# Performance work log

Measured on AMD Instinct MI355X. Metric: run time of the kernel, lower is better.

Reference implementation:

```python
import jax, jax.numpy as jnp
import numpy as np

V, E, H = 100000, 50, 64   # vocab, embedding dim, GRU hidden
B, T = 1024, 200           # batch, max playlist length


def setup_inputs() -> dict:
    key = jax.random.key(0)
    ks = jax.random.split(key, 12)
    ids = jax.random.randint(ks[0], (B, T), 1, V)
    lengths = jax.random.randint(ks[1], (B,), T // 4, T + 1)
    pos = jnp.arange(T)[None, :]
    input_tracks = jnp.where(pos < lengths[:, None], ids, 0)  # 0 = pad (mask_zero)
    s = 0.05
    p = lambda k, shp: jax.random.normal(k, shp, dtype=jnp.float32) * s
    z = lambda shp: jnp.zeros(shp, jnp.float32)
    return {
        "input_tracks": input_tracks,
        "emb": p(ks[2], (V, E)),
        "Wx_f": p(ks[3], (E, 3 * H)), "Wh_f": p(ks[4], (H, 3 * H)),
        "bi_f": z(3 * H), "br_f": z(3 * H),
        "Wx_b": p(ks[5], (E, 3 * H)), "Wh_b": p(ks[6], (H, 3 * H)),
        "bi_b": z(3 * H), "br_b": z(3 * H),
        "Wk": p(ks[7], (2 * H, H)), "bk": z(H),
        "Wq": p(ks[8], (H, H)), "bq": z(H),
        "We": p(ks[9], (H, 1)), "be": z(1),
    }


def _gru(x, mask, Wx, Wh, bi, br):
    """Keras GRU (reset_after=True) with masking; masked steps carry state.
    x: [B,T,E] float, mask: [B,T] bool. Returns (outputs [B,T,H], final state [B,H])."""
    gx = jnp.einsum('bte,eh->bth', x, Wx) + bi  # precompute input projections [B,T,3H]

    def step(h, inp):
        gxt, mt = inp                     # [B,3H], [B]
        gh = h @ Wh + br                  # [B,3H] recurrent projections (with recurrent bias)
        xz, xr, xh = jnp.split(gxt, 3, axis=-1)
        hz, hr, hn = jnp.split(gh, 3, axis=-1)
        zg = jax.nn.sigmoid(xz + hz)
        rg = jax.nn.sigmoid(xr + hr)
        hh = jnp.tanh(xh + rg * hn)
        h_new = zg * h + (1.0 - zg) * hh
        h_new = jnp.where(mt[:, None], h_new, h)  # carry state through padding
        return h_new, h_new

    h0 = jnp.zeros((x.shape[0], Wh.shape[0]), x.dtype)
    hT, outs = jax.lax.scan(step, h0, (gx.transpose(1, 0, 2), mask.T))
    return outs.transpose(1, 0, 2), hT


def reference(input_tracks, emb, Wx_f, Wh_f, bi_f, br_f, Wx_b, Wh_b, bi_b, br_b,
              Wk, bk, Wq, bq, We, be):
    mask = input_tracks != 0                       # [B,T]
    x = emb[input_tracks]                          # [B,T,E]
    out_f, h_f = _gru(x, mask, Wx_f, Wh_f, bi_f, br_f)
    out_b_rev, _ = _gru(x[:, ::-1], mask[:, ::-1], Wx_b, Wh_b, bi_b, br_b)
    out_b = out_b_rev[:, ::-1]
    out = jnp.concatenate([out_f, out_b], axis=-1)  # [B,T,2H]
    keys = out @ Wk + bk                            # [B,T,H]
    query = (h_f @ Wq + bq)[:, None, :]             # [B,1,H]
    energy = jnp.tanh(keys + query) @ We + be       # [B,T,1]
    energy = energy + (1.0 - mask.astype(jnp.float32))[:, :, None] * (-1e9)
    weights = jax.nn.softmax(energy, axis=1)        # softmax over time
    context = jnp.sum(weights * out, axis=1)        # [B,2H]
    return context
```

## Files before the change

### kernel.cpp

```cpp
#include <hip/hip_runtime.h>
#include <hip/hip_bf16.h>

#define VV 100000
#define EE 50
#define HH 64
#define BB 1024
#define TT 200

typedef float v4f __attribute__((ext_vector_type(4)));
typedef float f32x4 __attribute__((ext_vector_type(4)));
typedef short bf16x8 __attribute__((ext_vector_type(8)));
typedef _Float16 f16x8 __attribute__((ext_vector_type(8)));

__device__ __forceinline__ float fsig(float x) {
    return 1.f / (1.f + __expf(-x));
}
__device__ __forceinline__ float ftanh(float x) {
    float e = __expf(2.f * x);
    return 1.f - 2.f / (e + 1.f);
}
__device__ __forceinline__ short f2bf(float f) {
    union { float f; unsigned u; } v; v.f = f;
    unsigned r = v.u + 0x7FFFu + ((v.u >> 16) & 1u);
    return (short)(r >> 16);
}

__global__ __launch_bounds__(256) void embw_kernel(
    const float* __restrict__ emb,
    const float* __restrict__ Wx_f, const float* __restrict__ bi_f,
    const float* __restrict__ Wx_b, const float* __restrict__ bi_b,
    float* __restrict__ embW_f, float* __restrict__ embW_b)
{
    const float* Wx = blockIdx.y ? Wx_b : Wx_f;
    const float* bi = blockIdx.y ? bi_b : bi_f;
    float* embW     = blockIdx.y ? embW_b : embW_f;
    __shared__ float wx_lds[EE * 192];
    __shared__ float emb_lds[32 * EE];
    const int tid = threadIdx.x;
    const int v0 = blockIdx.x * 32;
    for (int i = tid; i < EE * 192; i += 256) wx_lds[i] = Wx[i];
    for (int i = tid; i < 32 * EE; i += 256) emb_lds[i] = emb[(size_t)v0 * EE + i];
    __syncthreads();
    const int cg = tid & 63;
    const int rg = tid >> 6;
    float acc[8][3];
    #pragma unroll
    for (int i = 0; i < 8; i++) {
        acc[i][0] = bi[cg];
        acc[i][1] = bi[cg + 64];
        acc[i][2] = bi[cg + 128];
    }
    for (int k = 0; k < EE; k++) {
        const float wx0 = wx_lds[k * 192 + cg];
        const float wx1 = wx_lds[k * 192 + cg + 64];
        const float wx2 = wx_lds[k * 192 + cg + 128];
        #pragma unroll
        for (int i = 0; i < 8; i++) {
            const float ev = emb_lds[(rg * 8 + i) * EE + k];
            acc[i][0] = fmaf(ev, wx0, acc[i][0]);
            acc[i][1] = fmaf(ev, wx1, acc[i][1]);
            acc[i][2] = fmaf(ev, wx2, acc[i][2]);
        }
    }
    #pragma unroll
    for (int i = 0; i < 8; i++) {
        const size_t row = (size_t)(v0 + rg * 8 + i) * 192;
        embW[row + cg]       = acc[i][0];
        embW[row + cg + 64]  = acc[i][1];
        embW[row + cg + 128] = acc[i][2];
    }
}

__global__ __launch_bounds__(256, 1) void gru8_kernel(
    const int* __restrict__ ids,
    const float* __restrict__ embW_f, const float* __restrict__ embW_b,
    const float* __restrict__ Wh_f, const float* __restrict__ br_f,
    const float* __restrict__ Wh_b, const float* __restrict__ br_b,
    float* __restrict__ outb,
    float* __restrict__ hf_out)
{
    const int tid  = threadIdx.x;
    const int w    = tid >> 6;
    const int lane = tid & 63;
    const int l15  = lane & 15;
    const int lhi  = lane >> 4;
    const int dir  = blockIdx.y;
    const int b0   = blockIdx.x * 16;
    const float* eW = dir ? embW_b : embW_f;
    const float* Wh = dir ? Wh_b : Wh_f;
    const float* br = dir ? br_b : br_f;
    const int c = 16 * w + l15;

    f16x8 bw[3][2];
    #pragma unroll
    for (int g = 0; g < 3; g++) {
        #pragma unroll
        for (int kt = 0; kt < 2; kt++) {
            #pragma unroll
            for (int jj = 0; jj < 8; jj++)
                bw[g][kt][jj] = (_Float16)Wh[(size_t)(32 * kt + 8 * lhi + jj) * 192 + 64 * g + c];
        }
    }
    const float brz = br[c], brr = br[64 + c], brn = br[128 + c];

    __shared__ __align__(16) _Float16 hlds[2][16][72];
    __shared__ int ids_s[16 * TT];
    for (int i = tid; i < 16 * TT; i += 256) ids_s[i] = ids[(size_t)b0 * TT + i];
    for (int i = tid; i < 2 * 16 * 72; i += 256) ((_Float16*)hlds)[i] = (_Float16)0.f;
    float hold[4] = {0.f, 0.f, 0.f, 0.f};
    __syncthreads();

    const int t0 = dir ? (TT - 1) : 0;
    const int dt = dir ? -1 : 1;

    int id0[4], id1[4];
    float gx0[3][4], gx1[3][4];
    #pragma unroll
    for (int r = 0; r < 4; r++) {
        id0[r] = ids_s[(4 * lhi + r) * TT + t0];
        id1[r] = ids_s[(4 * lhi + r) * TT + t0 + dt];
        const float* p0 = eW + (size_t)id0[r] * 192 + c;
        const float* p1 = eW + (size_t)id1[r] * 192 + c;
        #pragma unroll
        for (int g = 0; g < 3; g++) { gx0[g][r] = p0[64 * g]; gx1[g][r] = p1[64 * g]; }
    }

    int cur = 0;
    #pragma unroll 2
    for (int s = 0; s < TT; s++) {
        const int t = t0 + s * dt;
        int id2[4];
        float gx2[3][4];
        if (s + 2 < TT) {
            #pragma unroll
            for (int r = 0; r < 4; r++) {
                id2[r] = ids_s[(4 * lhi + r) * TT + t + 2 * dt];
                const float* p2 = eW + (size_t)id2[r] * 192 + c;
                #pragma unroll
                for (int g = 0; g < 3; g++) gx2[g][r] = p2[64 * g];
            }
        } else {
            #pragma unroll
            for (int r = 0; r < 4; r++) {
                id2[r] = 0;
                #pragma unroll
                for (int g = 0; g < 3; g++) gx2[g][r] = 0.f;
            }
        }
        const f16x8 a0 = *(const f16x8*)&hlds[cur][l15][8 * lhi];
        const f16x8 a1 = *(const f16x8*)&hlds[cur][l15][32 + 8 * lhi];
        f32x4 az = {0.f, 0.f, 0.f, 0.f};
        f32x4 ar = {0.f, 0.f, 0.f, 0.f};
        f32x4 an = {0.f, 0.f, 0.f, 0.f};
        az = __builtin_amdgcn_mfma_f32_16x16x32_f16(a0, bw[0][0], az, 0, 0, 0);
        ar = __builtin_amdgcn_mfma_f32_16x16x32_f16(a0, bw[1][0], ar, 0, 0, 0);
        an = __builtin_amdgcn_mfma_f32_16x16x32_f16(a0, bw[2][0], an, 0, 0, 0);
        az = __builtin_amdgcn_mfma_f32_16x16x32_f16(a1, bw[0][1], az, 0, 0, 0);
        ar = __builtin_amdgcn_mfma_f32_16x16x32_f16(a1, bw[1][1], ar, 0, 0, 0);
        an = __builtin_amdgcn_mfma_f32_16x16x32_f16(a1, bw[2][1], an, 0, 0, 0);
        #pragma unroll
        for (int r = 0; r < 4; r++) {
            const float z  = fsig(gx0[0][r] + az[r] + brz);
            const float rg = fsig(gx0[1][r] + ar[r] + brr);
            const float hh = ftanh(gx0[2][r] + rg * (an[r] + brn));
            float hnew = z * hold[r] + (1.f - z) * hh;
            hnew = (id0[r] != 0) ? hnew : hold[r];
            hold[r] = hnew;
            hlds[cur ^ 1][4 * lhi + r][c] = (_Float16)hnew;
            outb[((size_t)(b0 + 4 * lhi + r) * TT + t) * 128 + dir * 64 + c] = hnew;
        }
        cur ^= 1;
        asm volatile("s_waitcnt lgkmcnt(0)\n\ts_barrier" ::: "memory");
        #pragma unroll
        for (int r = 0; r < 4; r++) {
            id0[r] = id1[r]; id1[r] = id2[r];
            #pragma unroll
            for (int g = 0; g < 3; g++) { gx0[g][r] = gx1[g][r]; gx1[g][r] = gx2[g][r]; }
        }
    }
    if (dir == 0) {
        #pragma unroll
        for (int r = 0; r < 4; r++)
            hf_out[(size_t)(b0 + 4 * lhi + r) * 64 + c] = hold[r];
    }
}

#define NTILE 13

__global__ __launch_bounds__(256) void attn7_kernel(
    const int* __restrict__ ids,
    const float* __restrict__ outb,
    const float* __restrict__ hf,
    const float* __restrict__ Wk, const float* __restrict__ bk,
    const float* __restrict__ Wq, const float* __restrict__ bq,
    const float* __restrict__ We, const float* __restrict__ be,
    float* __restrict__ ctx)
{
    __shared__ __align__(16) short wk_sw[1024 * 8];
    __shared__ float q_lds[64];
    __shared__ float we_lds[64];
    __shared__ float e_lds[TT];
    __shared__ float part[4][128];
    const int b = blockIdx.x;
    const int tid = threadIdx.x;
    const int w = tid >> 6;
    const int lane = tid & 63;
    const int l15 = lane & 15;
    const int lhi = lane >> 4;

    #pragma unroll
    for (int i = 0; i < 4; i++) {
        const int slot = tid + 256 * i;
        const int s_l15 = slot & 15;
        const int s_nt  = (slot >> 4) & 3;
        const int s_lhi = (slot >> 6) & 3;
        const int s_ks  = slot >> 8;
        const int kbase = 32 * s_ks + 8 * s_lhi;
        const int col   = 16 * s_nt + s_l15;
        bf16x8 v;
        #pragma unroll
        for (int jj = 0; jj < 8; jj++) v[jj] = f2bf(Wk[(size_t)(kbase + jj) * 64 + col]);
        *(bf16x8*)&wk_sw[slot * 8] = v;
    }
    if (tid < 64) {
        float qc = bq[tid];
        const float* hfb = hf + (size_t)b * 64;
        for (int k = 0; k < 64; k++) qc = fmaf(hfb[k], Wq[k * 64 + tid], qc);
        q_lds[tid] = qc;
        we_lds[tid] = We[tid];
    }
    __syncthreads();

    for (int tile = w; tile < NTILE; tile += 4) {
        const int t0 = tile * 16;
        const int t = t0 + l15;
        f32x4 acc[4];
        #pragma unroll
        for (int nt = 0; nt < 4; nt++) { acc[nt][0] = 0.f; acc[nt][1] = 0.f; acc[nt][2] = 0.f; acc[nt][3] = 0.f; }
        #pragma unroll
        for (int ks = 0; ks < 4; ks++) {
            bf16x8 a;
            if (t < TT) {
                const float* p = outb + ((size_t)b * TT + t) * 128 + 32 * ks + 8 * lhi;
                const float4 lo = *(const float4*)p;
                const float4 hi = *(const float4*)(p + 4);
                a[0] = f2bf(lo.x); a[1] = f2bf(lo.y); a[2] = f2bf(lo.z); a[3] = f2bf(lo.w);
                a[4] = f2bf(hi.x); a[5] = f2bf(hi.y); a[6] = f2bf(hi.z); a[7] = f2bf(hi.w);
            } else {
                #pragma unroll
                for (int jj = 0; jj < 8; jj++) a[jj] = 0;
            }
            #pragma unroll
            for (int nt = 0; nt < 4; nt++) {
                const bf16x8 bf = *(const bf16x8*)&wk_sw[(ks * 256 + lhi * 64 + nt * 16 + l15) * 8];
                acc[nt] = __builtin_amdgcn_mfma_f32_16x16x32_bf16(a, bf, acc[nt], 0, 0, 0);
            }
        }
        float ep0 = 0.f, ep1 = 0.f, ep2 = 0.f, ep3 = 0.f;
        #pragma unroll
        for (int nt = 0; nt < 4; nt++) {
            const int c = 16 * nt + l15;
            const float qn = q_lds[c];
            const float wen = we_lds[c];
            ep0 = fmaf(wen, ftanh(acc[nt][0] + qn), ep0);
            ep1 = fmaf(wen, ftanh(acc[nt][1] + qn), ep1);
            ep2 = fmaf(wen, ftanh(acc[nt][2] + qn), ep2);
            ep3 = fmaf(wen, ftanh(acc[nt][3] + qn), ep3);
        }
        #pragma unroll
        for (int off = 1; off < 16; off <<= 1) {
            ep0 += __shfl_xor(ep0, off);
            ep1 += __shfl_xor(ep1, off);
            ep2 += __shfl_xor(ep2, off);
            ep3 += __shfl_xor(ep3, off);
        }
        if (l15 == 0) {
            const int rbase = t0 + 4 * lhi;
            if (rbase + 0 < TT) e_lds[rbase + 0] = ep0;
            if (rbase + 1 < TT) e_lds[rbase + 1] = ep1;
            if (rbase + 2 < TT) e_lds[rbase + 2] = ep2;
            if (rbase + 3 < TT) e_lds[rbase + 3] = ep3;
        }
    }
    __syncthreads();
    if (w == 0) {
        const float bev = be[0];
        for (int t = lane; t < TT; t += 64) {
            float e = e_lds[t] + bev;
            if (ids[(size_t)b * TT + t] == 0) e -= 1e9f;
            e_lds[t] = e;
        }
        float m = -1e30f;
        for (int t = lane; t < TT; t += 64) m = fmaxf(m, e_lds[t]);
        #pragma unroll
        for (int off = 32; off > 0; off >>= 1) m = fmaxf(m, __shfl_xor(m, off));
        float ssum = 0.f;
        for (int t = lane; t < TT; t += 64) { const float v = __expf(e_lds[t] - m); e_lds[t] = v; ssum += v; }
        #pragma unroll
        for (int off = 32; off > 0; off >>= 1) ssum += __shfl_xor(ssum, off);
        const float inv = 1.f / ssum;
        for (int t = lane; t < TT; t += 64) e_lds[t] *= inv;
    }
    __syncthreads();
    float c0 = 0.f, c1 = 0.f;
    for (int t = w; t < TT; t += 4) {
        const float* orow = outb + ((size_t)b * TT + t) * 128;
        const float wt = e_lds[t];
        c0 = fmaf(wt, orow[lane], c0);
        c1 = fmaf(wt, orow[64 + lane], c1);
    }
    part[w][lane] = c0;
    part[w][64 + lane] = c1;
    __syncthreads();
    if (tid < 128)
        ctx[(size_t)b * 128 + tid] = part[0][tid] + part[1][tid] + part[2][tid] + part[3][tid];
}

template<bool USE_EMBW>
__global__ __launch_bounds__(192, 2) void gru_kernel(
    const int* __restrict__ ids,
    const float* __restrict__ embW_f, const float* __restrict__ embW_b,
    const float* __restrict__ emb,
    const float* __restrict__ Wx_f, const float* __restrict__ bi_f,
    const float* __restrict__ Wx_b, const float* __restrict__ bi_b,
    const float* __restrict__ Wh_f, const float* __restrict__ br_f,
    const float* __restrict__ Wh_b, const float* __restrict__ br_b,
    float* __restrict__ outb, float* __restrict__ hf_out)
{
    constexpr int R = 4;
    __shared__ float h_lds[R][64];
    __shared__ float rg_lds[R][64];
    __shared__ float hh_lds[R][64];
    __shared__ int ids_lds[R * TT];
    const int tid = threadIdx.x;
    const int w = tid >> 6;
    const int j = tid & 63;
    const int dir = blockIdx.y;
    const int b0 = blockIdx.x * R;
    const float* embW = dir ? embW_b : embW_f;
    const float* Wh   = dir ? Wh_b : Wh_f;
    const float* br   = dir ? br_b : br_f;
    const float* Wx   = dir ? Wx_b : Wx_f;
    const float* bi   = dir ? bi_b : bi_f;
    const int c = w * 64 + j;

    float whc[64];
    #pragma unroll
    for (int k = 0; k < 64; k++) whc[k] = Wh[k * 192 + c];
    const float brc = br[c];
    float wxc[EE];
    float bic = 0.f;
    if (!USE_EMBW) {
        #pragma unroll
        for (int k = 0; k < EE; k++) wxc[k] = Wx[k * 192 + c];
        bic = bi[c];
    }
    for (int i = tid; i < R * TT; i += 192) ids_lds[i] = ids[(size_t)b0 * TT + i];
    if (w == 0) {
        #pragma unroll
        for (int r = 0; r < R; r++) h_lds[r][j] = 0.f;
    }
    __syncthreads();

    for (int s = 0; s < TT; s++) {
        const int t = dir ? (TT - 1 - s) : s;
        int idv[R];
        float gxv[R], accv[R];
        #pragma unroll
        for (int r = 0; r < R; r++) idv[r] = ids_lds[r * TT + t];
        if (USE_EMBW) {
            #pragma unroll
            for (int r = 0; r < R; r++) gxv[r] = embW[(size_t)idv[r] * 192 + c];
        } else {
            #pragma unroll
            for (int r = 0; r < R; r++) {
                float acc = bic;
                const float* er = emb + (size_t)idv[r] * EE;
                #pragma unroll
                for (int k = 0; k < EE; k++) acc = fmaf(er[k], wxc[k], acc);
                gxv[r] = acc;
            }
        }
        #pragma unroll
        for (int r = 0; r < R; r++) {
            float acc = brc;
            const float4* h4 = (const float4*)(&h_lds[r][0]);
            #pragma unroll
            for (int k4 = 0; k4 < 16; k4++) {
                const float4 hv = h4[k4];
                acc = fmaf(hv.x, whc[4 * k4 + 0], acc);
                acc = fmaf(hv.y, whc[4 * k4 + 1], acc);
                acc = fmaf(hv.z, whc[4 * k4 + 2], acc);
                acc = fmaf(hv.w, whc[4 * k4 + 3], acc);
            }
            accv[r] = acc;
        }
        float zg[R] = {};
        if (w == 1) {
            #pragma unroll
            for (int r = 0; r < R; r++) rg_lds[r][j] = fsig(gxv[r] + accv[r]);
        } else if (w == 0) {
            #pragma unroll
            for (int r = 0; r < R; r++) zg[r] = fsig(gxv[r] + accv[r]);
        }
        __syncthreads();
        if (w == 2) {
            #pragma unroll
            for (int r = 0; r < R; r++)
                hh_lds[r][j] = ftanh(gxv[r] + rg_lds[r][j] * accv[r]);
        }
        __syncthreads();
        if (w == 0) {
            #pragma unroll
            for (int r = 0; r < R; r++) {
                const float hold = h_lds[r][j];
                float hnew = hold;
                if (idv[r] != 0) {
                    const float hh = hh_lds[r][j];
                    hnew = zg[r] * hold + (1.f - zg[r]) * hh;
                }
                h_lds[r][j] = hnew;
                outb[((size_t)(b0 + r) * TT + t) * 128 + dir * 64 + j] = hnew;
            }
        }
        __syncthreads();
    }
    if (dir == 0 && w == 0) {
        #pragma unroll
        for (int r = 0; r < R; r++) hf_out[(size_t)(b0 + r) * 64 + j] = h_lds[r][j];
    }
}

extern "C" void kernel_launch(void* const* d_in, const int* in_sizes, int n_in,
                              void* d_out, int out_size, void* d_ws, size_t ws_size,
                              hipStream_t stream) {
    const int*   ids  = (const int*)d_in[0];
    const float* emb  = (const float*)d_in[1];
    const float* Wx_f = (const float*)d_in[2];
    const float* Wh_f = (const float*)d_in[3];
    const float* bi_f = (const float*)d_in[4];
    const float* br_f = (const float*)d_in[5];
    const float* Wx_b = (const float*)d_in[6];
    const float* Wh_b = (const float*)d_in[7];
    const float* bi_b = (const float*)d_in[8];
    const float* br_b = (const float*)d_in[9];
    const float* Wk   = (const float*)d_in[10];
    const float* bk   = (const float*)d_in[11];
    const float* Wq   = (const float*)d_in[12];
    const float* bq   = (const float*)d_in[13];
    const float* We   = (const float*)d_in[14];
    const float* be   = (const float*)d_in[15];
    float* ctx = (float*)d_out;

    float* ws = (float*)d_ws;
    const size_t embw_elems = (size_t)VV * 192;
    const size_t out_elems  = (size_t)BB * TT * 128;
    const size_t hf_elems   = (size_t)BB * 64;
    const size_t need_embw  = (2 * embw_elems + out_elems + hf_elems) * sizeof(float);
    const bool use_embw = (ws_size >= need_embw);

    float *embW_f = nullptr, *embW_b = nullptr, *outb, *hf;
    if (use_embw) {
        embW_f = ws;
        embW_b = embW_f + embw_elems;
        outb   = embW_b + embw_elems;
        hf     = outb + out_elems;
    } else {
        outb = ws;
        hf   = outb + out_elems;
    }

    if (use_embw) {
        embw_kernel<<<dim3(VV / 32, 2), 256, 0, stream>>>(
            emb, Wx_f, bi_f, Wx_b, bi_b, embW_f, embW_b);
        gru8_kernel<<<dim3(BB / 16, 2), 256, 0, stream>>>(
            ids, embW_f, embW_b, Wh_f, br_f, Wh_b, br_b, outb, hf);
    } else {
        gru_kernel<false><<<dim3(BB / 4, 2), 192, 0, stream>>>(
            ids, embW_f, embW_b, emb, Wx_f, bi_f, Wx_b, bi_b,
            Wh_f, br_f, Wh_b, br_b, outb, hf);
    }
    attn7_kernel<<<BB, 256, 0, stream>>>(ids, outb, hf, Wk, bk, Wq, bq, We, be, ctx);
}
```

Before: 327.2 us.

## Stage GRU input projections into LDS via async global_load_lds ring buffer

The GRU recurrence kernel now gathers the precomputed per-token input projections straight into a three-slot LDS ring buffer using global_load_lds, issued two steps ahead. This replaces the register-held prefetch of the same values. It also swaps the padded fp16 hidden-state buffer for an XOR-swizzled layout to avoid LDS bank conflicts. The goal is to take gather latency and VGPR pressure off the serial per-step critical path. In exchange it relies on a hand-written vmcnt wait count and a sched_barrier, and it uses more LDS.

```diff
diff --git a/kernel.cpp b/kernel.cpp
--- a/kernel.cpp
+++ b/kernel.cpp
@@ -71,7 +71,7 @@
     }
 }
 
-__global__ __launch_bounds__(256, 1) void gru8_kernel(
+__global__ __launch_bounds__(256, 1) void gru9_kernel(
     const int* __restrict__ ids,
     const float* __restrict__ embW_f, const float* __restrict__ embW_b,
     const float* __restrict__ Wh_f, const float* __restrict__ br_f,
@@ -103,52 +103,56 @@
     }
     const float brz = br[c], brr = br[64 + c], brn = br[128 + c];
 
-    __shared__ __align__(16) _Float16 hlds[2][16][72];
+    __shared__ float gx_s[3][16 * 193];
+    __shared__ __align__(16) char hbuf[2][2048];
     __shared__ int ids_s[16 * TT];
     for (int i = tid; i < 16 * TT; i += 256) ids_s[i] = ids[(size_t)b0 * TT + i];
-    for (int i = tid; i < 2 * 16 * 72; i += 256) ((_Float16*)hlds)[i] = (_Float16)0.f;
+    for (int i = tid; i < 1024; i += 256) ((unsigned*)hbuf)[i] = 0u;
     float hold[4] = {0.f, 0.f, 0.f, 0.f};
     __syncthreads();
 
     const int t0 = dir ? (TT - 1) : 0;
     const int dt = dir ? -1 : 1;
 
-    int id0[4], id1[4];
-    float gx0[3][4], gx1[3][4];
-    #pragma unroll
-    for (int r = 0; r < 4; r++) {
-        id0[r] = ids_s[(4 * lhi + r) * TT + t0];
-        id1[r] = ids_s[(4 * lhi + r) * TT + t0 + dt];
-        const float* p0 = eW + (size_t)id0[r] * 192 + c;
-        const float* p1 = eW + (size_t)id1[r] * 192 + c;
-        #pragma unroll
-        for (int g = 0; g < 3; g++) { gx0[g][r] = p0[64 * g]; gx1[g][r] = p1[64 * g]; }
-    }
-
+    #define STAGE(sl, tf)                                                                     \
+        {                                                                                     \
+            _Pragma("unroll")                                                                 \
+            for (int q = 0; q < 4; q++) {                                                     \
+                const int seqq = 4 * w + q;                                                   \
+                const int idq = ids_s[seqq * TT + (tf)];                                      \
+                const float* srcb = eW + (size_t)idq * 192;                                   \
+                _Pragma("unroll")                                                             \
+                for (int p = 0; p < 3; p++) {                                                 \
+                    __builtin_amdgcn_global_load_lds(                                         \
+                        (const __attribute__((address_space(1))) void*)(srcb + p * 64 + lane),\
+                        (__attribute__((address_space(3))) void*)(&gx_s[sl][seqq * 193 + p * 64]), \
+                        4, 0, 0);                                                             \
+                }                                                                             \
+            }                                                                                 \
+        }
+
+    STAGE(0, t0)
+    STAGE(1, t0 + dt)
+    __syncthreads();
+
+    int slot = 0;
+    int wslot = 2;
     int cur = 0;
-    #pragma unroll 2
+
     for (int s = 0; s < TT; s++) {
         const int t = t0 + s * dt;
-        int id2[4];
-        float gx2[3][4];
-        if (s + 2 < TT) {
-            #pragma unroll
-            for (int r = 0; r < 4; r++) {
-                id2[r] = ids_s[(4 * lhi + r) * TT + t + 2 * dt];
-                const float* p2 = eW + (size_t)id2[r] * 192 + c;
-                #pragma unroll
-                for (int g = 0; g < 3; g++) gx2[g][r] = p2[64 * g];
-            }
-        } else {
-            #pragma unroll
-            for (int r = 0; r < 4; r++) {
-                id2[r] = 0;
-                #pragma unroll
-                for (int g = 0; g < 3; g++) gx2[g][r] = 0.f;
-            }
-        }
-        const f16x8 a0 = *(const f16x8*)&hlds[cur][l15][8 * lhi];
-        const f16x8 a1 = *(const f16x8*)&hlds[cur][l15][32 + 8 * lhi];
+        int idv[4];
+        float gxv[3][4];
+        #pragma unroll
+        for (int r = 0; r < 4; r++) {
+            idv[r] = ids_s[(4 * lhi + r) * TT + t];
+            const float* base = &gx_s[slot][(4 * lhi + r) * 193 + c];
+            gxv[0][r] = base[0];
+            gxv[1][r] = base[64];
+            gxv[2][r] = base[128];
+        }
+        const f16x8 a0 = *(const f16x8*)(hbuf[cur] + l15 * 128 + ((lhi ^ (l15 & 7)) << 4));
+        const f16x8 a1 = *(const f16x8*)(hbuf[cur] + l15 * 128 + (((lhi + 4) ^ (l15 & 7)) << 4));
         f32x4 az = {0.f, 0.f, 0.f, 0.f};
         f32x4 ar = {0.f, 0.f, 0.f, 0.f};
         f32x4 an = {0.f, 0.f, 0.f, 0.f};
@@ -158,31 +162,33 @@
         az = __builtin_amdgcn_mfma_f32_16x16x32_f16(a1, bw[0][1], az, 0, 0, 0);
         ar = __builtin_amdgcn_mfma_f32_16x16x32_f16(a1, bw[1][1], ar, 0, 0, 0);
         an = __builtin_amdgcn_mfma_f32_16x16x32_f16(a1, bw[2][1], an, 0, 0, 0);
+        const int nxt = cur ^ 1;
         #pragma unroll
         for (int r = 0; r < 4; r++) {
-            const float z  = fsig(gx0[0][r] + az[r] + brz);
-            const float rg = fsig(gx0[1][r] + ar[r] + brr);
-            const float hh = ftanh(gx0[2][r] + rg * (an[r] + brn));
+            const float z  = fsig(gxv[0][r] + az[r] + brz);
+            const float rg = fsig(gxv[1][r] + ar[r] + brr);
+            const float hh = ftanh(gxv[2][r] + rg * (an[r] + brn));
             float hnew = z * hold[r] + (1.f - z) * hh;
-            hnew = (id0[r] != 0) ? hnew : hold[r];
+            hnew = (idv[r] != 0) ? hnew : hold[r];
             hold[r] = hnew;
-            hlds[cur ^ 1][4 * lhi + r][c] = (_Float16)hnew;
-            outb[((size_t)(b0 + 4 * lhi + r) * TT + t) * 128 + dir * 64 + c] = hnew;
-        }
-        cur ^= 1;
-        asm volatile("s_waitcnt lgkmcnt(0)\n\ts_barrier" ::: "memory");
-        #pragma unroll
-        for (int r = 0; r < 4; r++) {
-            id0[r] = id1[r]; id1[r] = id2[r];
-            #pragma unroll
-            for (int g = 0; g < 3; g++) { gx0[g][r] = gx1[g][r]; gx1[g][r] = gx2[g][r]; }
-        }
+            const int row = 4 * lhi + r;
+            const int wb = row * 128 + ((((c >> 3) ^ (row & 7))) << 4) + ((c & 7) << 1);
+            *(_Float16*)(hbuf[nxt] + wb) = (_Float16)hnew;
+            outb[((size_t)(b0 + row) * TT + t) * 128 + dir * 64 + c] = hnew;
+        }
+        cur = nxt;
+        if (s + 2 < TT) STAGE(wslot, t + 2 * dt)
+        asm volatile("s_waitcnt vmcnt(16) lgkmcnt(0)\n\ts_barrier" ::: "memory");
+        __builtin_amdgcn_sched_barrier(0);
+        slot = (slot == 2) ? 0 : slot + 1;
+        wslot = (wslot == 2) ? 0 : wslot + 1;
     }
     if (dir == 0) {
         #pragma unroll
         for (int r = 0; r < 4; r++)
             hf_out[(size_t)(b0 + 4 * lhi + r) * 64 + c] = hold[r];
     }
+    #undef STAGE
 }
 
 #define NTILE 13
@@ -473,7 +479,7 @@
     if (use_embw) {
         embw_kernel<<<dim3(VV / 32, 2), 256, 0, stream>>>(
             emb, Wx_f, bi_f, Wx_b, bi_b, embW_f, embW_b);
-        gru8_kernel<<<dim3(BB / 16, 2), 256, 0, stream>>>(
+        gru9_kernel<<<dim3(BB / 16, 2), 256, 0, stream>>>(
             ids, embW_f, embW_b, Wh_f, br_f, Wh_b, br_b, outb, hf);
     } else {
         gru_kernel<false><<<dim3(BB / 4, 2), 192, 0, stream>>>(
```

Result: slower. 335.5 us (+2.5%).

## Interleave both GRU directions per block with fp16 table and async LDS staging

Applied to the files above, without the earlier changes.

The precomputed embedding-times-Wx table is now stored in fp16, halving its memory footprint and the gather traffic. The GRU kernel runs forward and backward directions in the same block, interleaving their independent recurrences to hide latency, and halves the grid to 64 blocks. Per-step input gates are prefetched two steps ahead into a triple-buffered LDS ring via global_load_lds, and the hidden-state LDS buffer uses an XOR swizzle. The trade-offs are fewer blocks (64 on a many-CU GPU), more serial work per block, and lower precision in the input projections.

```diff
diff --git a/kernel.cpp b/kernel.cpp
--- a/kernel.cpp
+++ b/kernel.cpp
@@ -25,15 +25,15 @@
     return (short)(r >> 16);
 }
 
-__global__ __launch_bounds__(256) void embw_kernel(
+__global__ __launch_bounds__(256) void embw16_kernel(
     const float* __restrict__ emb,
     const float* __restrict__ Wx_f, const float* __restrict__ bi_f,
     const float* __restrict__ Wx_b, const float* __restrict__ bi_b,
-    float* __restrict__ embW_f, float* __restrict__ embW_b)
+    _Float16* __restrict__ embW_f, _Float16* __restrict__ embW_b)
 {
     const float* Wx = blockIdx.y ? Wx_b : Wx_f;
     const float* bi = blockIdx.y ? bi_b : bi_f;
-    float* embW     = blockIdx.y ? embW_b : embW_f;
+    _Float16* embW  = blockIdx.y ? embW_b : embW_f;
     __shared__ float wx_lds[EE * 192];
     __shared__ float emb_lds[32 * EE];
     const int tid = threadIdx.x;
@@ -65,15 +65,15 @@
     #pragma unroll
     for (int i = 0; i < 8; i++) {
         const size_t row = (size_t)(v0 + rg * 8 + i) * 192;
-        embW[row + cg]       = acc[i][0];
-        embW[row + cg + 64]  = acc[i][1];
-        embW[row + cg + 128] = acc[i][2];
-    }
-}
-
-__global__ __launch_bounds__(256, 1) void gru8_kernel(
+        embW[row + cg]       = (_Float16)acc[i][0];
+        embW[row + cg + 64]  = (_Float16)acc[i][1];
+        embW[row + cg + 128] = (_Float16)acc[i][2];
+    }
+}
+
+__global__ __launch_bounds__(256, 1) void gru10_kernel(
     const int* __restrict__ ids,
-    const float* __restrict__ embW_f, const float* __restrict__ embW_b,
+    const _Float16* __restrict__ eW_f, const _Float16* __restrict__ eW_b,
     const float* __restrict__ Wh_f, const float* __restrict__ br_f,
     const float* __restrict__ Wh_b, const float* __restrict__ br_b,
     float* __restrict__ outb,
@@ -84,105 +84,149 @@
     const int lane = tid & 63;
     const int l15  = lane & 15;
     const int lhi  = lane >> 4;
-    const int dir  = blockIdx.y;
     const int b0   = blockIdx.x * 16;
-    const float* eW = dir ? embW_b : embW_f;
-    const float* Wh = dir ? Wh_b : Wh_f;
-    const float* br = dir ? br_b : br_f;
     const int c = 16 * w + l15;
 
-    f16x8 bw[3][2];
+    f16x8 bwA[3][2], bwB[3][2];
     #pragma unroll
     for (int g = 0; g < 3; g++) {
         #pragma unroll
         for (int kt = 0; kt < 2; kt++) {
             #pragma unroll
-            for (int jj = 0; jj < 8; jj++)
-                bw[g][kt][jj] = (_Float16)Wh[(size_t)(32 * kt + 8 * lhi + jj) * 192 + 64 * g + c];
-        }
-    }
-    const float brz = br[c], brr = br[64 + c], brn = br[128 + c];
-
-    __shared__ __align__(16) _Float16 hlds[2][16][72];
+            for (int jj = 0; jj < 8; jj++) {
+                const size_t idx = (size_t)(32 * kt + 8 * lhi + jj) * 192 + 64 * g + c;
+                bwA[g][kt][jj] = (_Float16)Wh_f[idx];
+                bwB[g][kt][jj] = (_Float16)Wh_b[idx];
+            }
+        }
+    }
+    const float brA0 = br_f[c], brA1 = br_f[64 + c], brA2 = br_f[128 + c];
+    const float brB0 = br_b[c], brB1 = br_b[64 + c], brB2 = br_b[128 + c];
+
+    __shared__ _Float16 gxA_s[3][16 * 216];
+    __shared__ _Float16 gxB_s[3][16 * 216];
+    __shared__ __align__(16) char hbufA[2][2048];
+    __shared__ __align__(16) char hbufB[2][2048];
     __shared__ int ids_s[16 * TT];
+
     for (int i = tid; i < 16 * TT; i += 256) ids_s[i] = ids[(size_t)b0 * TT + i];
-    for (int i = tid; i < 2 * 16 * 72; i += 256) ((_Float16*)hlds)[i] = (_Float16)0.f;
-    float hold[4] = {0.f, 0.f, 0.f, 0.f};
-    __syncthreads();
-
-    const int t0 = dir ? (TT - 1) : 0;
-    const int dt = dir ? -1 : 1;
-
-    int id0[4], id1[4];
-    float gx0[3][4], gx1[3][4];
+    for (int i = tid; i < 1024; i += 256) { ((unsigned*)hbufA)[i] = 0u; ((unsigned*)hbufB)[i] = 0u; }
+    float holdA[4] = {0.f, 0.f, 0.f, 0.f};
+    float holdB[4] = {0.f, 0.f, 0.f, 0.f};
+    __syncthreads();
+
+    #define STAGE16(GX, EW, tf)                                                                  \
+        {                                                                                        \
+            _Pragma("unroll")                                                                    \
+            for (int q = 0; q < 4; q++) {                                                        \
+                const int seqq = 4 * w + q;                                                      \
+                const int idq = ids_s[seqq * TT + (tf)];                                         \
+                const _Float16* srcb = (EW) + (size_t)idq * 192 + lane * 2;                      \
+                __builtin_amdgcn_global_load_lds(                                                \
+                    (const __attribute__((address_space(1))) void*)srcb,                         \
+                    (__attribute__((address_space(3))) void*)(&(GX)[seqq * 216]), 4, 0, 0);      \
+                if (lane < 32)                                                                   \
+                    __builtin_amdgcn_global_load_lds(                                            \
+                        (const __attribute__((address_space(1))) void*)(srcb + 128),             \
+                        (__attribute__((address_space(3))) void*)(&(GX)[seqq * 216 + 128]), 4, 0, 0); \
+            }                                                                                    \
+        }
+
+    STAGE16(gxA_s[0], eW_f, 0)
+    STAGE16(gxB_s[0], eW_b, TT - 1)
+    STAGE16(gxA_s[1], eW_f, 1)
+    STAGE16(gxB_s[1], eW_b, TT - 2)
+    __syncthreads();
+
+    int slot = 0, wslot = 2, cur = 0;
+
+    for (int s = 0; s < TT; s++) {
+        const int tA = s;
+        const int tB = TT - 1 - s;
+        const int nxt = cur ^ 1;
+
+        {
+            int idv[4]; float gxv[3][4];
+            #pragma unroll
+            for (int r = 0; r < 4; r++) {
+                idv[r] = ids_s[(4 * lhi + r) * TT + tA];
+                #pragma unroll
+                for (int g = 0; g < 3; g++)
+                    gxv[g][r] = (float)gxA_s[slot][(4 * lhi + r) * 216 + 64 * g + c];
+            }
+            const f16x8 a0 = *(const f16x8*)(hbufA[cur] + l15 * 128 + ((lhi ^ (l15 & 7)) << 4));
+            const f16x8 a1 = *(const f16x8*)(hbufA[cur] + l15 * 128 + (((lhi + 4) ^ (l15 & 7)) << 4));
+            f32x4 az = {0.f, 0.f, 0.f, 0.f};
+            f32x4 ar = {0.f, 0.f, 0.f, 0.f};
+            f32x4 an = {0.f, 0.f, 0.f, 0.f};
+            az = __builtin_amdgcn_mfma_f32_16x16x32_f16(a0, bwA[0][0], az, 0, 0, 0);
+            ar = __builtin_amdgcn_mfma_f32_16x16x32_f16(a0, bwA[1][0], ar, 0, 0, 0);
+            an = __builtin_amdgcn_mfma_f32_16x16x32_f16(a0, bwA[2][0], an, 0, 0, 0);
+            az = __builtin_amdgcn_mfma_f32_16x16x32_f16(a1, bwA[0][1], az, 0, 0, 0);
+            ar = __builtin_amdgcn_mfma_f32_16x16x32_f16(a1, bwA[1][1], ar, 0, 0, 0);
+            an = __builtin_amdgcn_mfma_f32_16x16x32_f16(a1, bwA[2][1], an, 0, 0, 0);
+            #pragma unroll
+            for (int r = 0; r < 4; r++) {
+                const float z  = fsig(gxv[0][r] + az[r] + brA0);
+                const float rg = fsig(gxv[1][r] + ar[r] + brA1);
+                const float hh = ftanh(gxv[2][r] + rg * (an[r] + brA2));
+                float hnew = hh + z * (holdA[r] - hh);
+                hnew = (idv[r] != 0) ? hnew : holdA[r];
+                holdA[r] = hnew;
+                const int row = 4 * lhi + r;
+                const int wb = row * 128 + (((c >> 3) ^ (row & 7)) << 4) + ((c & 7) << 1);
+                *(_Float16*)(hbufA[nxt] + wb) = (_Float16)hnew;
+                outb[((size_t)(b0 + row) * TT + tA) * 128 + c] = hnew;
+            }
+        }
+        {
+            int idv[4]; float gxv[3][4];
+            #pragma unroll
+            for (int r = 0; r < 4; r++) {
+                idv[r] = ids_s[(4 * lhi + r) * TT + tB];
+                #pragma unroll
+                for (int g = 0; g < 3; g++)
+                    gxv[g][r] = (float)gxB_s[slot][(4 * lhi + r) * 216 + 64 * g + c];
+            }
+            const f16x8 a0 = *(const f16x8*)(hbufB[cur] + l15 * 128 + ((lhi ^ (l15 & 7)) << 4));
+            const f16x8 a1 = *(const f16x8*)(hbufB[cur] + l15 * 128 + (((lhi + 4) ^ (l15 & 7)) << 4));
+            f32x4 az = {0.f, 0.f, 0.f, 0.f};
+            f32x4 ar = {0.f, 0.f, 0.f, 0.f};
+            f32x4 an = {0.f, 0.f, 0.f, 0.f};
+            az = __builtin_amdgcn_mfma_f32_16x16x32_f16(a0, bwB[0][0], az, 0, 0, 0);
+            ar = __builtin_amdgcn_mfma_f32_16x16x32_f16(a0, bwB[1][0], ar, 0, 0, 0);
+            an = __builtin_amdgcn_mfma_f32_16x16x32_f16(a0, bwB[2][0], an, 0, 0, 0);
+            az = __builtin_amdgcn_mfma_f32_16x16x32_f16(a1, bwB[0][1], az, 0, 0, 0);
+            ar = __builtin_amdgcn_mfma_f32_16x16x32_f16(a1, bwB[1][1], ar, 0, 0, 0);
+            an = __builtin_amdgcn_mfma_f32_16x16x32_f16(a1, bwB[2][1], an, 0, 0, 0);
+            #pragma unroll
+            for (int r = 0; r < 4; r++) {
+                const float z  = fsig(gxv[0][r] + az[r] + brB0);
+                const float rg = fsig(gxv[1][r] + ar[r] + brB1);
+                const float hh = ftanh(gxv[2][r] + rg * (an[r] + brB2));
+                float hnew = hh + z * (holdB[r] - hh);
+                hnew = (idv[r] != 0) ? hnew : holdB[r];
+                holdB[r] = hnew;
+                const int row = 4 * lhi + r;
+                const int wb = row * 128 + (((c >> 3) ^ (row & 7)) << 4) + ((c & 7) << 1);
+                *(_Float16*)(hbufB[nxt] + wb) = (_Float16)hnew;
+                outb[((size_t)(b0 + row) * TT + tB) * 128 + 64 + c] = hnew;
+            }
+        }
+        cur = nxt;
+        if (s + 2 < TT) {
+            STAGE16(gxA_s[wslot], eW_f, s + 2)
+            STAGE16(gxB_s[wslot], eW_b, TT - 3 - s)
+        }
+        asm volatile("s_waitcnt vmcnt(24) lgkmcnt(0)\n\ts_barrier" ::: "memory");
+        __builtin_amdgcn_sched_barrier(0);
+        slot = (slot == 2) ? 0 : slot + 1;
+        wslot = (wslot == 2) ? 0 : wslot + 1;
+    }
     #pragma unroll
-    for (int r = 0; r < 4; r++) {
-        id0[r] = ids_s[(4 * lhi + r) * TT + t0];
-        id1[r] = ids_s[(4 * lhi + r) * TT + t0 + dt];
-        const float* p0 = eW + (size_t)id0[r] * 192 + c;
-        const float* p1 = eW + (size_t)id1[r] * 192 + c;
-        #pragma unroll
-        for (int g = 0; g < 3; g++) { gx0[g][r] = p0[64 * g]; gx1[g][r] = p1[64 * g]; }
-    }
-
-    int cur = 0;
-    #pragma unroll 2
-    for (int s = 0; s < TT; s++) {
-        const int t = t0 + s * dt;
-        int id2[4];
-        float gx2[3][4];
-        if (s + 2 < TT) {
-            #pragma unroll
-            for (int r = 0; r < 4; r++) {
-                id2[r] = ids_s[(4 * lhi + r) * TT + t + 2 * dt];
-                const float* p2 = eW + (size_t)id2[r] * 192 + c;
-                #pragma unroll
-                for (int g = 0; g < 3; g++) gx2[g][r] = p2[64 * g];
-            }
-        } else {
-            #pragma unroll
-            for (int r = 0; r < 4; r++) {
-                id2[r] = 0;
-                #pragma unroll
-                for (int g = 0; g < 3; g++) gx2[g][r] = 0.f;
-            }
-        }
-        const f16x8 a0 = *(const f16x8*)&hlds[cur][l15][8 * lhi];
-        const f16x8 a1 = *(const f16x8*)&hlds[cur][l15][32 + 8 * lhi];
-        f32x4 az = {0.f, 0.f, 0.f, 0.f};
-        f32x4 ar = {0.f, 0.f, 0.f, 0.f};
-        f32x4 an = {0.f, 0.f, 0.f, 0.f};
-        az = __builtin_amdgcn_mfma_f32_16x16x32_f16(a0, bw[0][0], az, 0, 0, 0);
-        ar = __builtin_amdgcn_mfma_f32_16x16x32_f16(a0, bw[1][0], ar, 0, 0, 0);
-        an = __builtin_amdgcn_mfma_f32_16x16x32_f16(a0, bw[2][0], an, 0, 0, 0);
-        az = __builtin_amdgcn_mfma_f32_16x16x32_f16(a1, bw[0][1], az, 0, 0, 0);
-        ar = __builtin_amdgcn_mfma_f32_16x16x32_f16(a1, bw[1][1], ar, 0, 0, 0);
-        an = __builtin_amdgcn_mfma_f32_16x16x32_f16(a1, bw[2][1], an, 0, 0, 0);
-        #pragma unroll
-        for (int r = 0; r < 4; r++) {
-            const float z  = fsig(gx0[0][r] + az[r] + brz);
-            const float rg = fsig(gx0[1][r] + ar[r] + brr);
-            const float hh = ftanh(gx0[2][r] + rg * (an[r] + brn));
-            float hnew = z * hold[r] + (1.f - z) * hh;
-            hnew = (id0[r] != 0) ? hnew : hold[r];
-            hold[r] = hnew;
-            hlds[cur ^ 1][4 * lhi + r][c] = (_Float16)hnew;
-            outb[((size_t)(b0 + 4 * lhi + r) * TT + t) * 128 + dir * 64 + c] = hnew;
-        }
-        cur ^= 1;
-        asm volatile("s_waitcnt lgkmcnt(0)\n\ts_barrier" ::: "memory");
-        #pragma unroll
-        for (int r = 0; r < 4; r++) {
-            id0[r] = id1[r]; id1[r] = id2[r];
-            #pragma unroll
-            for (int g = 0; g < 3; g++) { gx0[g][r] = gx1[g][r]; gx1[g][r] = gx2[g][r]; }
-        }
-    }
-    if (dir == 0) {
-        #pragma unroll
-        for (int r = 0; r < 4; r++)
-            hf_out[(size_t)(b0 + 4 * lhi + r) * 64 + c] = hold[r];
-    }
+    for (int r = 0; r < 4; r++)
+        hf_out[(size_t)(b0 + 4 * lhi + r) * 64 + c] = holdA[r];
+    #undef STAGE16
 }
 
 #define NTILE 13
@@ -452,33 +496,28 @@
     const float* be   = (const float*)d_in[15];
     float* ctx = (float*)d_out;
 
-    float* ws = (float*)d_ws;
     const size_t embw_elems = (size_t)VV * 192;
     const size_t out_elems  = (size_t)BB * TT * 128;
     const size_t hf_elems   = (size_t)BB * 64;
-    const size_t need_embw  = (2 * embw_elems + out_elems + hf_elems) * sizeof(float);
-    const bool use_embw = (ws_size >= need_embw);
-
-    float *embW_f = nullptr, *embW_b = nullptr, *outb, *hf;
+    const size_t need = embw_elems * 2 * sizeof(_Float16) + (out_elems + hf_elems) * sizeof(float);
+    const bool use_embw = (ws_size >= need);
+
     if (use_embw) {
-        embW_f = ws;
-        embW_b = embW_f + embw_elems;
-        outb   = embW_b + embw_elems;
-        hf     = outb + out_elems;
+        _Float16* embW16_f = (_Float16*)d_ws;
+        _Float16* embW16_b = embW16_f + embw_elems;
+        float* outb = (float*)(embW16_b + embw_elems);
+        float* hf   = outb + out_elems;
+        embw16_kernel<<<dim3(VV / 32, 2), 256, 0, stream>>>(
+            emb, Wx_f, bi_f, Wx_b, bi_b, embW16_f, embW16_b);
+        gru10_kernel<<<BB / 16, 256, 0, stream>>>(
+            ids, embW16_f, embW16_b, Wh_f, br_f, Wh_b, br_b, outb, hf);
+        attn7_kernel<<<BB, 256, 0, stream>>>(ids, outb, hf, Wk, bk, Wq, bq, We, be, ctx);
     } else {
-        outb = ws;
-        hf   = outb + out_elems;
-    }
-
-    if (use_embw) {
-        embw_kernel<<<dim3(VV / 32, 2), 256, 0, stream>>>(
-            emb, Wx_f, bi_f, Wx_b, bi_b, embW_f, embW_b);
-        gru8_kernel<<<dim3(BB / 16, 2), 256, 0, stream>>>(
-            ids, embW_f, embW_b, Wh_f, br_f, Wh_b, br_b, outb, hf);
-    } else {
+        float* outb = (float*)d_ws;
+        float* hf   = outb + out_elems;
         gru_kernel<false><<<dim3(BB / 4, 2), 192, 0, stream>>>(
-            ids, embW_f, embW_b, emb, Wx_f, bi_f, Wx_b, bi_b,
+            ids, nullptr, nullptr, emb, Wx_f, bi_f, Wx_b, bi_b,
             Wh_f, br_f, Wh_b, br_b, outb, hf);
-    }
-    attn7_kernel<<<BB, 256, 0, stream>>>(ids, outb, hf, Wk, bk, Wq, bq, We, be, ctx);
-}
+        attn7_kernel<<<BB, 256, 0, stream>>>(ids, outb, hf, Wk, bk, Wq, bq, We, be, ctx);
+    }
+}
```

Measured after the change: 553.0 us. 1.69x slower.
